# Performance work log

Measured on AMD Instinct MI355X. Metric: run time of the kernel, lower is better.

The kernel has to match this reference:

```python
import jax, jax.numpy as jnp
import numpy as np

B, T, D, H = 8, 1024, 1024, 16
NEG = -1e9  # stands in for -inf in the causal mask (matches float('-inf') semantics under softmax)


def setup_inputs() -> dict:
    key = jax.random.key(0)
    ks = jax.random.split(key, 8)
    s = 0.02
    x = jax.random.normal(ks[0], (B, T, D), dtype=jnp.float32)
    # additive causal mask like whisper: zeros on/below diagonal, -inf above
    mask = jnp.triu(jnp.full((T, T), NEG, dtype=jnp.float32), k=1)
    Wq = jax.random.normal(ks[1], (D, D), dtype=jnp.float32) * s
    bq = jax.random.normal(ks[2], (D,), dtype=jnp.float32) * s
    Wk = jax.random.normal(ks[3], (D, D), dtype=jnp.float32) * s
    Wv = jax.random.normal(ks[4], (D, D), dtype=jnp.float32) * s
    bv = jax.random.normal(ks[5], (D,), dtype=jnp.float32) * s
    Wo = jax.random.normal(ks[6], (D, D), dtype=jnp.float32) * s
    bo = jax.random.normal(ks[7], (D,), dtype=jnp.float32) * s
    return {"x": x, "mask": mask, "Wq": Wq, "bq": bq, "Wk": Wk, "Wv": Wv, "bv": bv, "Wo": Wo, "bo": bo}


def reference(x, mask, Wq, bq, Wk, Wv, bv, Wo, bo):
    n_batch, n_ctx, n_state = x.shape
    head_dim = n_state // H
    scale = head_dim ** (-0.25)

    q = x @ Wq.T + bq            # [B,T,D]
    k = x @ Wk.T                 # key Linear has no bias
    v = x @ Wv.T + bv

    # [B,T,D] -> [B,H,T,hd]
    q = q.reshape(n_batch, n_ctx, H, head_dim).transpose(0, 2, 1, 3) * scale
    kt = k.reshape(n_batch, n_ctx, H, head_dim).transpose(0, 2, 3, 1) * scale  # [B,H,hd,T]
    v = v.reshape(n_batch, n_ctx, H, head_dim).transpose(0, 2, 1, 3)

    qk = jnp.einsum('bhqd,bhdk->bhqk', q, kt) + mask[:n_ctx, :n_ctx]
    w = jax.nn.softmax(qk.astype(jnp.float32), axis=-1).astype(q.dtype)
    wv = jnp.einsum('bhqk,bhkd->bhqd', w, v)  # [B,H,T,hd]
    wv = wv.transpose(0, 2, 1, 3).reshape(n_batch, n_ctx, n_state)
    return wv @ Wo.T + bo
```

## Files before the change

### kernel.cpp

```cpp
#include <hip/hip_runtime.h>
#include <stdint.h>

typedef unsigned short u16;
typedef __attribute__((ext_vector_type(8))) short bf16x8;
typedef __attribute__((ext_vector_type(4))) float f32x4;

__device__ __forceinline__ float b2f(u16 u) {
    union { uint32_t i; float f; } c; c.i = ((uint32_t)u) << 16; return c.f;
}
__device__ __forceinline__ u16 f2b(float f) {
    union { float f; uint32_t i; } c; c.f = f;
    uint32_t u = c.i;
    uint32_t r = (u + 0x7fffu + ((u >> 16) & 1u)) >> 16;
    return (u16)r;
}
__device__ __forceinline__ uint32_t fbits(float f) {
    union { float f; uint32_t u; } c; c.f = f; return c.u;
}

__device__ __forceinline__ void gll16(const u16* g, u16* lds_base) {
    __builtin_amdgcn_global_load_lds(
        (const __attribute__((address_space(1))) uint32_t*)g,
        (__attribute__((address_space(3))) uint32_t*)lds_base, 16, 0, 0);
}

#define GK 1024
#define QSCALE 0.18033688011112042f
#define LDPA 72

__global__ __launch_bounds__(256) void conv_all(
    const void* x, const void* wq, const void* bqp, const void* wk,
    const void* wv, const void* bvp, const void* wo, const void* bop,
    u16* xb, u16* wqb, u16* bqb, u16* wkb, u16* wvb, u16* bvb, u16* wob, u16* bob,
    const u16* __restrict__ sniff)
{
    const bool is_f32 = (sniff[1] == 0);
    const int blk = blockIdx.x;
    const void* s; u16* d; int i0, n;
    if (blk < 4096)      { s = x;   d = xb;  i0 = blk;        n = 8388608; }
    else if (blk < 4608) { s = wq;  d = wqb; i0 = blk - 4096; n = 1048576; }
    else if (blk < 5120) { s = wk;  d = wkb; i0 = blk - 4608; n = 1048576; }
    else if (blk < 5632) { s = wv;  d = wvb; i0 = blk - 5120; n = 1048576; }
    else if (blk < 6144) { s = wo;  d = wob; i0 = blk - 5632; n = 1048576; }
    else if (blk == 6144){ s = bqp; d = bqb; i0 = 0;          n = 1024; }
    else if (blk == 6145){ s = bvp; d = bvb; i0 = 0;          n = 1024; }
    else                 { s = bop; d = bob; i0 = 0;          n = 1024; }
    int i = (i0 * 256 + threadIdx.x) * 8;
    if (i >= n) return;
    if (is_f32) {
        const float* sf = (const float*)s;
        float4 lo = *(const float4*)(sf + i);
        float4 hi = *(const float4*)(sf + i + 4);
        u16 o[8];
        o[0]=f2b(lo.x); o[1]=f2b(lo.y); o[2]=f2b(lo.z); o[3]=f2b(lo.w);
        o[4]=f2b(hi.x); o[5]=f2b(hi.y); o[6]=f2b(hi.z); o[7]=f2b(hi.w);
        *(uint4*)(d + i) = *(const uint4*)o;
    } else {
        *(uint4*)(d + i) = *(const uint4*)((const u16*)s + i);
    }
}


#define VM6 asm volatile("s_waitcnt vmcnt(6)" ::: "memory")
#define VM4 asm volatile("s_waitcnt vmcnt(4)" ::: "memory")
#define VM0 asm volatile("s_waitcnt vmcnt(0)" ::: "memory")
#define BARR do { __builtin_amdgcn_s_barrier(); asm volatile("" ::: "memory"); } while(0)

#define PHASE(Q, BUF, DO_STAGE, UU)                                            \
  {                                                                            \
    const u16* Sa = &S[(((BUF) << 2) | (((Q) >> 1) << 1))][0];                 \
    bf16x8 af0 = *(const bf16x8*)(Sa + aoff[((Q)&1)*4 + 0]);                   \
    bf16x8 af1 = *(const bf16x8*)(Sa + aoff[((Q)&1)*4 + 1]);                   \
    bf16x8 af2 = *(const bf16x8*)(Sa + aoff[((Q)&1)*4 + 2]);                   \
    bf16x8 af3 = *(const bf16x8*)(Sa + aoff[((Q)&1)*4 + 3]);                   \
    if (((Q) & 1) == 0) {                                                      \
      const u16* Sbp = Sa + 8192;                                              \
      bfr[0] = *(const bf16x8*)(Sbp + boff[0]);                                \
      bfr[1] = *(const bf16x8*)(Sbp + boff[1]);                                \
      bfr[2] = *(const bf16x8*)(Sbp + boff[2]);                                \
      bfr[3] = *(const bf16x8*)(Sbp + boff[3]);                                \
    }                                                                          \
    if (DO_STAGE) STAGE(UU);                                                   \
    asm volatile("s_waitcnt lgkmcnt(0)" ::: "memory");                         \
    __builtin_amdgcn_sched_barrier(0);                                         \
    __builtin_amdgcn_s_setprio(1);                                             \
    _Pragma("unroll")                                                          \
    for (int jj = 0; jj < 4; jj++) {                                           \
      acc[((Q)&1)*4+0][jj] = __builtin_amdgcn_mfma_f32_16x16x32_bf16(af0, bfr[jj], acc[((Q)&1)*4+0][jj], 0,0,0); \
      acc[((Q)&1)*4+1][jj] = __builtin_amdgcn_mfma_f32_16x16x32_bf16(af1, bfr[jj], acc[((Q)&1)*4+1][jj], 0,0,0); \
      acc[((Q)&1)*4+2][jj] = __builtin_amdgcn_mfma_f32_16x16x32_bf16(af2, bfr[jj], acc[((Q)&1)*4+2][jj], 0,0,0); \
      acc[((Q)&1)*4+3][jj] = __builtin_amdgcn_mfma_f32_16x16x32_bf16(af3, bfr[jj], acc[((Q)&1)*4+3][jj], 0,0,0); \
    }                                                                          \
    __builtin_amdgcn_s_setprio(0);                                             \
  }

__global__ __launch_bounds__(512, 2) void gemm_qkv(
    const u16* __restrict__ xb, const u16* __restrict__ wcomb,
    const u16* __restrict__ bq, const u16* __restrict__ bv,
    u16* __restrict__ qb, u16* __restrict__ kb, u16* __restrict__ vtb)
{
    __shared__ __align__(16) u16 S[8][8192];

    const int flat = blockIdx.x;
    const int xcd = flat & 7, pos = flat >> 3;
    const int mt = xcd * 4 + (pos & 3);
    const int nt = pos >> 2;
    const int m0 = mt * 256;
    const int n0 = nt * 256;

    const int tid = threadIdx.x;
    const int lane = tid & 63, w = tid >> 6;
    const int quad = lane >> 4, l15 = lane & 15;
    const int wm = w >> 2, wn = w & 3;

    const int srow = tid >> 2;
    const int chk = (tid & 3) ^ ((tid >> 3) & 3);
    const u16* pA1 = xb    + (size_t)(m0 + srow) * GK + chk * 8;
    const u16* pA2 = xb    + (size_t)(m0 + 128 + srow) * GK + chk * 8;
    const u16* pB1 = wcomb + (size_t)(n0 + srow) * GK + chk * 8;
    const u16* pB2 = wcomb + (size_t)(n0 + 128 + srow) * GK + chk * 8;

    const int cq = (quad ^ ((l15 >> 1) & 3)) * 8;
    int aoff[8], boff[4];
#pragma unroll
    for (int mf = 0; mf < 8; mf++)
        aoff[mf] = (wm * 128 + mf * 16 + l15) * 32 + cq;
#pragma unroll
    for (int nf = 0; nf < 4; nf++)
        boff[nf] = (wn * 64 + nf * 16 + l15) * 32 + cq;

    f32x4 acc[8][4];
#pragma unroll
    for (int i = 0; i < 8; i++)
#pragma unroll
        for (int j = 0; j < 4; j++)
            acc[i][j] = (f32x4){0.f, 0.f, 0.f, 0.f};
    bf16x8 bfr[4];

    auto STAGE = [&](int U) {
        const int tau = U >> 2, ty = U & 3;
        const int ko = tau * 64 + (ty >> 1) * 32;
        u16* d = &S[((tau & 1) << 2) | ty][w * 512];
        const u16* s1 = (ty & 1) ? pB1 : pA1;
        const u16* s2 = (ty & 1) ? pB2 : pA2;
        gll16(s1 + ko, d);
        gll16(s2 + ko, d + 4096);
    };

    STAGE(0); STAGE(1); STAGE(2); STAGE(3); STAGE(4);
    VM6; BARR;

#pragma unroll 1
    for (int it = 0; it < 14; ++it) {
        const int buf = it & 1;
        const int U0 = it * 4 + 5;
        PHASE(0, buf, true, U0);           BARR;
        PHASE(1, buf, true, U0 + 1);  VM6; BARR;
        PHASE(2, buf, true, U0 + 2);       BARR;
        PHASE(3, buf, true, U0 + 3);  VM6; BARR;
    }
    PHASE(0, 0, true, 61);       BARR;
    PHASE(1, 0, true, 62);  VM6; BARR;
    PHASE(2, 0, true, 63);       BARR;
    PHASE(3, 0, false, 0);  VM4; BARR;
    PHASE(0, 1, false, 0);       BARR;
    PHASE(1, 1, false, 0);  VM0; BARR;
    PHASE(2, 1, false, 0);       BARR;
    PHASE(3, 1, false, 0);

    const int which = nt >> 2;
    const int nbase = (nt & 3) * 256 + wn * 64;
#pragma unroll
    for (int mi = 0; mi < 8; mi++)
#pragma unroll
        for (int ni = 0; ni < 4; ni++) {
            const int gn = nbase + ni * 16 + l15;
            const int gm = m0 + wm * 128 + mi * 16 + quad * 4;
            if (which == 2) {
                const int b = gm >> 10, ml = gm & 1023;
                const int h = gn >> 6, dw = gn & 63;
                const float bb = b2f(bv[gn]);
                union { u16 h4[4]; uint2 v; } pk;
#pragma unroll
                for (int r = 0; r < 4; r++)
                    pk.h4[r] = f2b(acc[mi][ni][r] + bb);
                *(uint2*)(vtb + (((size_t)(b * 16 + h) * 64 + dw) << 10) + ml) = pk.v;
            } else if (which == 0) {
                const float bb = b2f(bq[gn]);
#pragma unroll
                for (int r = 0; r < 4; r++)
                    qb[(size_t)(gm + r) * 1024 + gn] = f2b((acc[mi][ni][r] + bb) * QSCALE);
            } else {
#pragma unroll
                for (int r = 0; r < 4; r++)
                    kb[(size_t)(gm + r) * 1024 + gn] = f2b(acc[mi][ni][r]);
            }
        }
}

__global__ __launch_bounds__(512, 2) void gemm_out(
    const u16* __restrict__ A, const u16* __restrict__ W,
    const u16* __restrict__ bias, float* __restrict__ C)
{
    __shared__ __align__(16) u16 S[8][8192];

    const int flat = blockIdx.x;
    const int xcd = flat & 7, pos = flat >> 3;
    const int mt = xcd * 4 + (pos & 3);
    const int nt = pos >> 2;
    const int m0 = mt * 256;
    const int n0 = nt * 256;

    const int tid = threadIdx.x;
    const int lane = tid & 63, w = tid >> 6;
    const int quad = lane >> 4, l15 = lane & 15;
    const int wm = w >> 2, wn = w & 3;

    const int srow = tid >> 2;
    const int chk = (tid & 3) ^ ((tid >> 3) & 3);
    const u16* pA1 = A + (size_t)(m0 + srow) * GK + chk * 8;
    const u16* pA2 = A + (size_t)(m0 + 128 + srow) * GK + chk * 8;
    const u16* pB1 = W + (size_t)(n0 + srow) * GK + chk * 8;
    const u16* pB2 = W + (size_t)(n0 + 128 + srow) * GK + chk * 8;

    const int cq = (quad ^ ((l15 >> 1) & 3)) * 8;
    int aoff[8], boff[4];
#pragma unroll
    for (int mf = 0; mf < 8; mf++)
        aoff[mf] = (wm * 128 + mf * 16 + l15) * 32 + cq;
#pragma unroll
    for (int nf = 0; nf < 4; nf++)
        boff[nf] = (wn * 64 + nf * 16 + l15) * 32 + cq;

    f32x4 acc[8][4];
#pragma unroll
    for (int i = 0; i < 8; i++)
#pragma unroll
        for (int j = 0; j < 4; j++)
            acc[i][j] = (f32x4){0.f, 0.f, 0.f, 0.f};
    bf16x8 bfr[4];

    auto STAGE = [&](int U) {
        const int tau = U >> 2, ty = U & 3;
        const int ko = tau * 64 + (ty >> 1) * 32;
        u16* d = &S[((tau & 1) << 2) | ty][w * 512];
        const u16* s1 = (ty & 1) ? pB1 : pA1;
        const u16* s2 = (ty & 1) ? pB2 : pA2;
        gll16(s1 + ko, d);
        gll16(s2 + ko, d + 4096);
    };

    STAGE(0); STAGE(1); STAGE(2); STAGE(3); STAGE(4);
    VM6; BARR;

#pragma unroll 1
    for (int it = 0; it < 14; ++it) {
        const int buf = it & 1;
        const int U0 = it * 4 + 5;
        PHASE(0, buf, true, U0);           BARR;
        PHASE(1, buf, true, U0 + 1);  VM6; BARR;
        PHASE(2, buf, true, U0 + 2);       BARR;
        PHASE(3, buf, true, U0 + 3);  VM6; BARR;
    }
    PHASE(0, 0, true, 61);       BARR;
    PHASE(1, 0, true, 62);  VM6; BARR;
    PHASE(2, 0, true, 63);       BARR;
    PHASE(3, 0, false, 0);  VM4; BARR;
    PHASE(0, 1, false, 0);       BARR;
    PHASE(1, 1, false, 0);  VM0; BARR;
    PHASE(2, 1, false, 0);       BARR;
    PHASE(3, 1, false, 0);

#pragma unroll
    for (int mi = 0; mi < 8; mi++)
#pragma unroll
        for (int ni = 0; ni < 4; ni++) {
            const int gn = n0 + wn * 64 + ni * 16 + l15;
            const int gm = m0 + wm * 128 + mi * 16 + quad * 4;
            const float bb = b2f(bias[gn]);
#pragma unroll
            for (int r = 0; r < 4; r++)
                C[(size_t)(gm + r) * 1024 + gn] = acc[mi][ni][r] + bb;
        }
}

__global__ __launch_bounds__(512, 4) void attn_kernel(
    const u16* q, const u16* kg, const u16* vt, u16* o)
{
    const int qt = (blockIdx.x + 2 * (blockIdx.y >> 6)) & 3;
    const int bh = blockIdx.y;
    const int b = bh >> 4, h = bh & 15;
    const size_t base = (size_t)b * 1024 * 1024 + (size_t)h * 64;
    const size_t vbase = (size_t)bh * 64 * 1024;

    __shared__ __align__(16) u16 Ks[2][64 * LDPA];
    __shared__ __align__(16) u16 Vs[2][64 * LDPA];
    __shared__ __align__(16) u16 U[256 * LDPA];

    const int t = threadIdx.x;
    const int lane = t & 63, w = t >> 6;
    const int quad = lane >> 4, l15 = lane & 15;

#pragma unroll
    for (int i = 0; i < 4; i++) {
        int idx = i * 512 + t;
        int r = idx >> 3, c = idx & 7;
        *(uint4*)(&U[r * LDPA + c * 8]) =
            *(const uint4*)(q + base + (size_t)(qt * 256 + r) * 1024 + c * 8);
    }
    __syncthreads();
    bf16x8 qf[2][2];
#pragma unroll
    for (int qc = 0; qc < 2; qc++)
#pragma unroll
        for (int ks = 0; ks < 2; ks++)
            qf[qc][ks] = *(const bf16x8*)(&U[(w * 32 + qc * 16 + l15) * LDPA + ks * 32 + quad * 8]);
    __syncthreads();
    u16* Pw = &U[(w * 32) * LDPA];

    const int wqmin = qt * 256 + w * 32;
    float l_[2] = {0.f, 0.f};
    f32x4 accO[2][4];
#pragma unroll
    for (int qc = 0; qc < 2; qc++)
#pragma unroll
        for (int f = 0; f < 4; f++) accO[qc][f] = (f32x4){0.f, 0.f, 0.f, 0.f};

    const int jmax = 4 * qt + 3;
    const int sr = t >> 3, sc = (t & 7) * 8;
    uint4 rK = *(const uint4*)(kg + base + (size_t)sr * 1024 + sc);
    uint4 rV = *(const uint4*)(vt + vbase + (size_t)sr * 1024 + sc);

    for (int j = 0; j <= jmax; j++) {
        const int buf = j & 1;
        *(uint4*)(&Ks[buf][sr * LDPA + sc]) = rK;
        *(uint4*)(&Vs[buf][sr * LDPA + sc]) = rV;
        if (j < jmax) {
            rK = *(const uint4*)(kg + base + (size_t)((j + 1) * 64 + sr) * 1024 + sc);
            rV = *(const uint4*)(vt + vbase + (size_t)sr * 1024 + (j + 1) * 64 + sc);
        }
        __syncthreads();

        if (j * 64 > wqmin + 31) continue;

        f32x4 st[2][4];
#pragma unroll
        for (int qc = 0; qc < 2; qc++)
#pragma unroll
            for (int ni = 0; ni < 4; ni++) st[qc][ni] = (f32x4){0.f, 0.f, 0.f, 0.f};
#pragma unroll
        for (int ks = 0; ks < 2; ks++)
#pragma unroll
            for (int ni = 0; ni < 4; ni++) {
                bf16x8 kf = *(const bf16x8*)(&Ks[buf][(ni * 16 + l15) * LDPA + ks * 32 + quad * 8]);
                st[0][ni] = __builtin_amdgcn_mfma_f32_16x16x32_bf16(kf, qf[0][ks], st[0][ni], 0, 0, 0);
                st[1][ni] = __builtin_amdgcn_mfma_f32_16x16x32_bf16(kf, qf[1][ks], st[1][ni], 0, 0, 0);
            }

        const bool diag = (j * 64 + 63 > wqmin);
#pragma unroll
        for (int qc = 0; qc < 2; qc++) {
            const int q_g = wqmin + qc * 16 + l15;
            float ps = 0.f;
#pragma unroll
            for (int ni = 0; ni < 4; ni++) {
                float p[4];
#pragma unroll
                for (int r = 0; r < 4; r++) {
                    float e = __builtin_amdgcn_exp2f(st[qc][ni][r]);
                    if (diag) {
                        int key_g = j * 64 + ni * 16 + quad * 4 + r;
                        e = (key_g > q_g) ? 0.f : e;
                    }
                    p[r] = e;
                    ps += e;
                }
                uint2 pkv;
                pkv.x = __builtin_amdgcn_perm(fbits(p[1]) + 0x8000u, fbits(p[0]) + 0x8000u, 0x07060302u);
                pkv.y = __builtin_amdgcn_perm(fbits(p[3]) + 0x8000u, fbits(p[2]) + 0x8000u, 0x07060302u);
                *(uint2*)(&Pw[(qc * 16 + l15) * LDPA + ni * 16 + quad * 4]) = pkv;
            }
            l_[qc] += ps;
        }

#pragma unroll
        for (int ks = 0; ks < 2; ks++) {
            bf16x8 pf0 = *(const bf16x8*)(&Pw[(l15) * LDPA + ks * 32 + quad * 8]);
            bf16x8 pf1 = *(const bf16x8*)(&Pw[(16 + l15) * LDPA + ks * 32 + quad * 8]);
#pragma unroll
            for (int f = 0; f < 4; f++) {
                bf16x8 vf = *(const bf16x8*)(&Vs[buf][(f * 16 + l15) * LDPA + ks * 32 + quad * 8]);
                accO[0][f] = __builtin_amdgcn_mfma_f32_16x16x32_bf16(vf, pf0, accO[0][f], 0, 0, 0);
                accO[1][f] = __builtin_amdgcn_mfma_f32_16x16x32_bf16(vf, pf1, accO[1][f], 0, 0, 0);
            }
        }
    }

#pragma unroll
    for (int qc = 0; qc < 2; qc++) {
        float l = l_[qc];
        l += __shfl_xor(l, 16, 64);
        l += __shfl_xor(l, 32, 64);
        float inv = 1.0f / l;
        const int q_g = wqmin + qc * 16 + l15;
#pragma unroll
        for (int f = 0; f < 4; f++) {
            union { u16 h4[4]; uint2 v; } pk;
#pragma unroll
            for (int r = 0; r < 4; r++) pk.h4[r] = f2b(accO[qc][f][r] * inv);
            *(uint2*)(o + base + (size_t)q_g * 1024 + f * 16 + quad * 4) = pk.v;
        }
    }
}

extern "C" void kernel_launch(void* const* d_in, const int* in_sizes, int n_in,
                              void* d_out, int out_size, void* d_ws, size_t ws_size,
                              hipStream_t stream) {
    const u16* mask = (const u16*)d_in[1];

    const size_t MT = (size_t)8192 * 1024;
    const size_t WT = (size_t)1024 * 1024;
    u16* ws  = (u16*)d_ws;
    u16* xb  = ws;
    u16* qb  = xb + MT;
    u16* kb  = qb + MT;
    u16* vtb = kb + MT;
    u16* wqb = vtb + MT;
    u16* wkb = wqb + WT;
    u16* wvb = wkb + WT;
    u16* wob = wvb + WT;
    u16* bqb = wob + WT;
    u16* bvb = bqb + 1024;
    u16* bob = bvb + 1024;

    hipLaunchKernelGGL(conv_all, dim3(6147), dim3(256), 0, stream,
                       d_in[0], d_in[2], d_in[3], d_in[4], d_in[5], d_in[6],
                       d_in[7], d_in[8],
                       xb, wqb, bqb, wkb, wvb, bvb, wob, bob, mask);

    hipLaunchKernelGGL(gemm_qkv, dim3(384), dim3(512), 0, stream,
                       xb, wqb, bqb, bvb, qb, kb, vtb);

    hipLaunchKernelGGL(attn_kernel, dim3(4, 128), dim3(512), 0, stream, qb, kb, vtb, qb);

    hipLaunchKernelGGL(gemm_out, dim3(128), dim3(512), 0, stream,
                       qb, wob, bob, (float*)d_out);
}
```

Before: 244.1 us.

## Retile output GEMM to 128x128 triple-buffered, reschedule QKV barriers, load Q directly

The output projection GEMM moves from 256x256 tiles with 512 threads to 128x128 tiles with 256 threads and a 3-stage LDS ring. This quadruples the grid to 512 blocks so more CUs stay busy. The QKV GEMM now waits on loads and hits the barrier before the MFMA block in each phase instead of after it. The attention kernel reads Q fragments straight from global memory instead of staging them through LDS with two syncthreads, and uses a different per-head query-tile ordering. Smaller tiles give less data reuse per block, and the earlier barrier placement could reduce overlap.

Result: faster. 232.7 us (-4.7%).

```diff
diff --git a/kernel.cpp b/kernel.cpp
--- a/kernel.cpp
+++ b/kernel.cpp
@@ -64,9 +64,10 @@
 #define VM6 asm volatile("s_waitcnt vmcnt(6)" ::: "memory")
 #define VM4 asm volatile("s_waitcnt vmcnt(4)" ::: "memory")
 #define VM0 asm volatile("s_waitcnt vmcnt(0)" ::: "memory")
+#define VMN asm volatile("" ::: "memory")
 #define BARR do { __builtin_amdgcn_s_barrier(); asm volatile("" ::: "memory"); } while(0)
 
-#define PHASE(Q, BUF, DO_STAGE, UU)                                            \
+#define PHASE(Q, BUF, DO_STAGE, UU, VMW)                                       \
   {                                                                            \
     const u16* Sa = &S[(((BUF) << 2) | (((Q) >> 1) << 1))][0];                 \
     bf16x8 af0 = *(const bf16x8*)(Sa + aoff[((Q)&1)*4 + 0]);                   \
@@ -81,6 +82,8 @@
       bfr[3] = *(const bf16x8*)(Sbp + boff[3]);                                \
     }                                                                          \
     if (DO_STAGE) STAGE(UU);                                                   \
+    VMW;                                                                       \
+    __builtin_amdgcn_s_barrier();                                              \
     asm volatile("s_waitcnt lgkmcnt(0)" ::: "memory");                         \
     __builtin_amdgcn_sched_barrier(0);                                         \
     __builtin_amdgcn_s_setprio(1);                                             \
@@ -154,19 +157,19 @@
     for (int it = 0; it < 14; ++it) {
         const int buf = it & 1;
         const int U0 = it * 4 + 5;
-        PHASE(0, buf, true, U0);           BARR;
-        PHASE(1, buf, true, U0 + 1);  VM6; BARR;
-        PHASE(2, buf, true, U0 + 2);       BARR;
-        PHASE(3, buf, true, U0 + 3);  VM6; BARR;
+        PHASE(0, buf, true, U0,     VM6);
+        PHASE(1, buf, true, U0 + 1, VM6);
+        PHASE(2, buf, true, U0 + 2, VMN);
+        PHASE(3, buf, true, U0 + 3, VM6);
     }
-    PHASE(0, 0, true, 61);       BARR;
-    PHASE(1, 0, true, 62);  VM6; BARR;
-    PHASE(2, 0, true, 63);       BARR;
-    PHASE(3, 0, false, 0);  VM4; BARR;
-    PHASE(0, 1, false, 0);       BARR;
-    PHASE(1, 1, false, 0);  VM0; BARR;
-    PHASE(2, 1, false, 0);       BARR;
-    PHASE(3, 1, false, 0);
+    PHASE(0, 0, true, 61, VM6);
+    PHASE(1, 0, true, 62, VM6);
+    PHASE(2, 0, true, 63, VMN);
+    PHASE(3, 0, false, 0, VM4);
+    PHASE(0, 1, false, 0, VMN);
+    PHASE(1, 1, false, 0, VM0);
+    PHASE(2, 1, false, 0, VMN);
+    PHASE(3, 1, false, 0, VMN);
 
     const int which = nt >> 2;
     const int nbase = (nt & 3) * 256 + wn * 64;
@@ -198,85 +201,98 @@
         }
 }
 
-__global__ __launch_bounds__(512, 2) void gemm_out(
+__global__ __launch_bounds__(256, 3) void gemm_out(
     const u16* __restrict__ A, const u16* __restrict__ W,
     const u16* __restrict__ bias, float* __restrict__ C)
 {
-    __shared__ __align__(16) u16 S[8][8192];
+    __shared__ __align__(16) u16 S[3][8192];
 
     const int flat = blockIdx.x;
     const int xcd = flat & 7, pos = flat >> 3;
-    const int mt = xcd * 4 + (pos & 3);
-    const int nt = pos >> 2;
-    const int m0 = mt * 256;
-    const int n0 = nt * 256;
-
-    const int tid = threadIdx.x;
-    const int lane = tid & 63, w = tid >> 6;
+    const int mt = xcd * 8 + (pos & 7);
+    const int nt = pos >> 3;
+    const int m0 = mt * 128;
+    const int n0 = nt * 128;
+
+    const int t = threadIdx.x;
+    const int lane = t & 63, w = t >> 6;
     const int quad = lane >> 4, l15 = lane & 15;
-    const int wm = w >> 2, wn = w & 3;
-
-    const int srow = tid >> 2;
-    const int chk = (tid & 3) ^ ((tid >> 3) & 3);
-    const u16* pA1 = A + (size_t)(m0 + srow) * GK + chk * 8;
-    const u16* pA2 = A + (size_t)(m0 + 128 + srow) * GK + chk * 8;
-    const u16* pB1 = W + (size_t)(n0 + srow) * GK + chk * 8;
-    const u16* pB2 = W + (size_t)(n0 + 128 + srow) * GK + chk * 8;
+    const int wm = w >> 1, wn = w & 1;
+
+    const int srow = lane >> 2;
+    const int gs = (lane & 3) ^ ((lane >> 3) & 3);
+    const u16* srcA0 = A + (size_t)(m0 + w * 16 + srow) * GK + gs * 8;
+    const u16* srcA1 = A + (size_t)(m0 + 64 + w * 16 + srow) * GK + gs * 8;
+    const u16* srcB0 = W + (size_t)(n0 + w * 16 + srow) * GK + gs * 8;
+    const u16* srcB1 = W + (size_t)(n0 + 64 + w * 16 + srow) * GK + gs * 8;
 
     const int cq = (quad ^ ((l15 >> 1) & 3)) * 8;
-    int aoff[8], boff[4];
-#pragma unroll
-    for (int mf = 0; mf < 8; mf++)
-        aoff[mf] = (wm * 128 + mf * 16 + l15) * 32 + cq;
-#pragma unroll
-    for (int nf = 0; nf < 4; nf++)
-        boff[nf] = (wn * 64 + nf * 16 + l15) * 32 + cq;
-
-    f32x4 acc[8][4];
-#pragma unroll
-    for (int i = 0; i < 8; i++)
+    int aoff[4], boff[4];
+#pragma unroll
+    for (int mi = 0; mi < 4; mi++)
+        aoff[mi] = (wm * 64 + mi * 16 + l15) * 32 + cq;
+#pragma unroll
+    for (int ni = 0; ni < 4; ni++)
+        boff[ni] = 4096 + (wn * 64 + ni * 16 + l15) * 32 + cq;
+
+    f32x4 acc[4][4];
+#pragma unroll
+    for (int i = 0; i < 4; i++)
 #pragma unroll
         for (int j = 0; j < 4; j++)
             acc[i][j] = (f32x4){0.f, 0.f, 0.f, 0.f};
-    bf16x8 bfr[4];
-
-    auto STAGE = [&](int U) {
-        const int tau = U >> 2, ty = U & 3;
-        const int ko = tau * 64 + (ty >> 1) * 32;
-        u16* d = &S[((tau & 1) << 2) | ty][w * 512];
-        const u16* s1 = (ty & 1) ? pB1 : pA1;
-        const u16* s2 = (ty & 1) ? pB2 : pA2;
-        gll16(s1 + ko, d);
-        gll16(s2 + ko, d + 4096);
+
+    auto STAGE = [&](int h) {
+        u16* Sn = &S[h % 3][0];
+        const int ko = h * 32;
+        gll16(srcA0 + ko, Sn + w * 512);
+        gll16(srcA1 + ko, Sn + 2048 + w * 512);
+        gll16(srcB0 + ko, Sn + 4096 + w * 512);
+        gll16(srcB1 + ko, Sn + 6144 + w * 512);
     };
-
-    STAGE(0); STAGE(1); STAGE(2); STAGE(3); STAGE(4);
-    VM6; BARR;
-
-#pragma unroll 1
-    for (int it = 0; it < 14; ++it) {
-        const int buf = it & 1;
-        const int U0 = it * 4 + 5;
-        PHASE(0, buf, true, U0);           BARR;
-        PHASE(1, buf, true, U0 + 1);  VM6; BARR;
-        PHASE(2, buf, true, U0 + 2);       BARR;
-        PHASE(3, buf, true, U0 + 3);  VM6; BARR;
+    auto KSTEP = [&](int h, bool doStage) {
+        const u16* Sb = &S[h % 3][0];
+        bf16x8 af[4], bf[4];
+#pragma unroll
+        for (int mi = 0; mi < 4; mi++) af[mi] = *(const bf16x8*)(Sb + aoff[mi]);
+#pragma unroll
+        for (int ni = 0; ni < 4; ni++) bf[ni] = *(const bf16x8*)(Sb + boff[ni]);
+        if (doStage) STAGE(h + 2);
+        asm volatile("s_waitcnt lgkmcnt(0)" ::: "memory");
+        __builtin_amdgcn_sched_barrier(0);
+        __builtin_amdgcn_s_setprio(1);
+#pragma unroll
+        for (int mi = 0; mi < 4; mi++)
+#pragma unroll
+            for (int ni = 0; ni < 4; ni++)
+                acc[mi][ni] = __builtin_amdgcn_mfma_f32_16x16x32_bf16(
+                    af[mi], bf[ni], acc[mi][ni], 0, 0, 0);
+        __builtin_amdgcn_s_setprio(0);
+    };
+
+    STAGE(0); STAGE(1);
+    asm volatile("s_waitcnt vmcnt(4)" ::: "memory");
+    __builtin_amdgcn_s_barrier();
+    asm volatile("" ::: "memory");
+
+    for (int h = 0; h < 30; ++h) {
+        KSTEP(h, true);
+        asm volatile("s_waitcnt vmcnt(4)" ::: "memory");
+        __builtin_amdgcn_s_barrier();
+        asm volatile("" ::: "memory");
     }
-    PHASE(0, 0, true, 61);       BARR;
-    PHASE(1, 0, true, 62);  VM6; BARR;
-    PHASE(2, 0, true, 63);       BARR;
-    PHASE(3, 0, false, 0);  VM4; BARR;
-    PHASE(0, 1, false, 0);       BARR;
-    PHASE(1, 1, false, 0);  VM0; BARR;
-    PHASE(2, 1, false, 0);       BARR;
-    PHASE(3, 1, false, 0);
-
-#pragma unroll
-    for (int mi = 0; mi < 8; mi++)
+    KSTEP(30, false);
+    asm volatile("s_waitcnt vmcnt(0)" ::: "memory");
+    __builtin_amdgcn_s_barrier();
+    asm volatile("" ::: "memory");
+    KSTEP(31, false);
+
+#pragma unroll
+    for (int mi = 0; mi < 4; mi++)
 #pragma unroll
         for (int ni = 0; ni < 4; ni++) {
             const int gn = n0 + wn * 64 + ni * 16 + l15;
-            const int gm = m0 + wm * 128 + mi * 16 + quad * 4;
+            const int gm = m0 + wm * 64 + mi * 16 + quad * 4;
             const float bb = b2f(bias[gn]);
 #pragma unroll
             for (int r = 0; r < 4; r++)
@@ -287,7 +303,8 @@
 __global__ __launch_bounds__(512, 4) void attn_kernel(
     const u16* q, const u16* kg, const u16* vt, u16* o)
 {
-    const int qt = (blockIdx.x + 2 * (blockIdx.y >> 6)) & 3;
+    const int qt0 = blockIdx.x & 3;
+    const int qt = ((blockIdx.y >> 6) & 1) ? (qt0 ^ 3) : qt0;
     const int bh = blockIdx.y;
     const int b = bh >> 4, h = bh & 15;
     const size_t base = (size_t)b * 1024 * 1024 + (size_t)h * 64;
@@ -301,21 +318,13 @@
     const int lane = t & 63, w = t >> 6;
     const int quad = lane >> 4, l15 = lane & 15;
 
-#pragma unroll
-    for (int i = 0; i < 4; i++) {
-        int idx = i * 512 + t;
-        int r = idx >> 3, c = idx & 7;
-        *(uint4*)(&U[r * LDPA + c * 8]) =
-            *(const uint4*)(q + base + (size_t)(qt * 256 + r) * 1024 + c * 8);
-    }
-    __syncthreads();
     bf16x8 qf[2][2];
 #pragma unroll
     for (int qc = 0; qc < 2; qc++)
 #pragma unroll
         for (int ks = 0; ks < 2; ks++)
-            qf[qc][ks] = *(const bf16x8*)(&U[(w * 32 + qc * 16 + l15) * LDPA + ks * 32 + quad * 8]);
-    __syncthreads();
+            qf[qc][ks] = *(const bf16x8*)(q + base +
+                (size_t)(qt * 256 + w * 32 + qc * 16 + l15) * 1024 + ks * 32 + quad * 8);
     u16* Pw = &U[(w * 32) * LDPA];
 
     const int wqmin = qt * 256 + w * 32;
@@ -443,6 +452,6 @@
 
     hipLaunchKernelGGL(attn_kernel, dim3(4, 128), dim3(512), 0, stream, qb, kb, vtb, qb);
 
-    hipLaunchKernelGGL(gemm_out, dim3(128), dim3(512), 0, stream,
+    hipLaunchKernelGGL(gemm_out, dim3(512), dim3(256), 0, stream,
                        qb, wob, bob, (float*)d_out);
 }
```
